# Optimization experiments

Hardware: AMD Instinct MI355X
Metric: run time of the kernel (lower is better)

Reference implementation:

```python
import jax, jax.numpy as jnp
import numpy as np

N0, N1, N2 = 100000, 20000, 4000
E0, E1 = 500000, 100000
D_IN, D_HID, D_OUT = 256, 256, 256


def setup_inputs() -> dict:
    key = jax.random.key(0)
    ks = jax.random.split(key, 12)
    s = 1.0 / np.sqrt(D_IN)
    return {
        "x": jax.random.normal(ks[0], (N0, D_IN), jnp.float32),
        "src0": jax.random.randint(ks[1], (E0,), 0, N0, jnp.int32),
        "dst0": jax.random.randint(ks[2], (E0,), 0, N1, jnp.int32),
        "w0": jax.random.uniform(ks[3], (E0,), jnp.float32),
        "src1": jax.random.randint(ks[4], (E1,), 0, N1, jnp.int32),
        "dst1": jax.random.randint(ks[5], (E1,), 0, N2, jnp.int32),
        "w1": jax.random.uniform(ks[6], (E1,), jnp.float32),
        "Wp1": jax.random.normal(ks[7], (D_IN, D_IN), jnp.float32) * s,
        "bp1": jnp.zeros((D_IN,), jnp.float32),
        "Ws1": jax.random.normal(ks[8], (D_IN, D_HID), jnp.float32) * s,
        "Wn1": jax.random.normal(ks[9], (D_IN, D_HID), jnp.float32) * s,
        "b1": jnp.zeros((D_HID,), jnp.float32),
        "Wp2": jax.random.normal(ks[10], (D_HID, D_HID), jnp.float32) * s,
        "bp2": jnp.zeros((D_HID,), jnp.float32),
        "Ws2": jax.random.normal(ks[11], (D_HID, D_OUT), jnp.float32) * s,
        "Wn2": jax.random.normal(jax.random.fold_in(key, 99), (D_HID, D_OUT), jnp.float32) * s,
        "b2": jnp.zeros((D_OUT,), jnp.float32),
    }


def sage_pool(x_src, src, dst, w, Wp, bp, Ws, Wn, b, n_dst):
    # DGL SAGEConv 'pool': relu(fc_pool(src feats)), edge-weighted msg, max reduce
    h = jax.nn.relu(x_src @ Wp + bp)          # [Nsrc, d]
    msg = h[src] * w[:, None]                 # [E, d] gather + edge weight
    agg = jax.ops.segment_max(msg, dst, num_segments=n_dst)
    agg = jnp.where(jnp.isfinite(agg), agg, 0.0)  # zero for isolated dst nodes
    x_dst = x_src[:n_dst]                     # block convention: dst = first n_dst src
    return x_dst @ Ws + agg @ Wn + b


def reference(x, src0, dst0, w0, src1, dst1, w1,
              Wp1, bp1, Ws1, Wn1, b1, Wp2, bp2, Ws2, Wn2, b2):
    h = sage_pool(x, src0, dst0, w0, Wp1, bp1, Ws1, Wn1, b1, N1)
    h = jax.nn.relu(h)
    h = sage_pool(h, src1, dst1, w1, Wp2, bp2, Ws2, Wn2, b2, N2)
    return jax.nn.relu(h)
```

## Files before the change

### kernel.cpp

```cpp
#include <hip/hip_runtime.h>
#include <hip/hip_bf16.h>

#define D 256
#define N0C 100000
#define N1C 20000
#define N2C 4000
#define BCAP 64
#define OVFCAP 4096

typedef short s16x8 __attribute__((ext_vector_type(8)));
typedef float f32x4 __attribute__((ext_vector_type(4)));

typedef __attribute__((address_space(3))) void lds_v;
typedef __attribute__((address_space(1))) void glb_v;

__device__ __forceinline__ short f2bf(float f) {
  __hip_bfloat16 b = __float2bfloat16(f);
  union { __hip_bfloat16 h; short s; } u;
  u.h = b;
  return u.s;
}
__device__ __forceinline__ float bf2f(short s) {
  return __uint_as_float(((unsigned)(unsigned short)s) << 16);
}

__global__ __launch_bounds__(256) void wtransp_k(
    const float* __restrict__ W0, const float* __restrict__ W1,
    const float* __restrict__ W2, const float* __restrict__ W3,
    const float* __restrict__ W4, const float* __restrict__ W5,
    short* __restrict__ T0, short* __restrict__ T1, short* __restrict__ T2,
    short* __restrict__ T3, short* __restrict__ T4, short* __restrict__ T5,
    int* __restrict__ ctrs, int nctr)
{
  int flat = (blockIdx.y * gridDim.x + blockIdx.x) * 256 + threadIdx.x;
  if (flat < nctr) ctrs[flat] = 0;

  const float* Ws[6] = {W0, W1, W2, W3, W4, W5};
  short* Ts[6] = {T0, T1, T2, T3, T4, T5};
  int g = blockIdx.y;
  int c = blockIdx.x * 256 + threadIdx.x;
  int lane = c & 63, kc = (c >> 6) & 7, g16 = c >> 9;
  int col = g16 * 16 + (lane & 15);
  int kbase = kc * 32 + (lane >> 4) * 8;
  const float* W = Ws[g];
  s16x8 o;
#pragma unroll
  for (int j = 0; j < 8; ++j) o[j] = f2bf(W[(size_t)(kbase + j) * D + col]);
  *(s16x8*)(Ts[g] + (size_t)c * 8) = o;
}

__global__ __launch_bounds__(256) void scat_direct_k(
    const int* __restrict__ src0, const int* __restrict__ dst0,
    const float* __restrict__ w0, int E0, int* __restrict__ cur0,
    int2* __restrict__ rec0, int* __restrict__ ovfc0, int4* __restrict__ ovf0,
    const int* __restrict__ src1, const int* __restrict__ dst1,
    const float* __restrict__ w1, int E1, int* __restrict__ cur1,
    int2* __restrict__ rec1, int* __restrict__ ovfc1, int4* __restrict__ ovf1)
{
  int i = blockIdx.x * 256 + threadIdx.x;
  if (i < E0) {
    int d = dst0[i];
    int p = atomicAdd(&cur0[d], 1);
    if (p < BCAP) rec0[d * BCAP + p] = make_int2(src0[i], __float_as_int(w0[i]));
    else {
      int q = atomicAdd(ovfc0, 1);
      if (q < OVFCAP) ovf0[q] = make_int4(d, src0[i], __float_as_int(w0[i]), 0);
    }
  } else if (i < E0 + E1) {
    int j = i - E0;
    int d = dst1[j];
    int p = atomicAdd(&cur1[d], 1);
    if (p < BCAP) rec1[d * BCAP + p] = make_int2(src1[j], __float_as_int(w1[j]));
    else {
      int q = atomicAdd(ovfc1, 1);
      if (q < OVFCAP) ovf1[q] = make_int4(d, src1[j], __float_as_int(w1[j]), 0);
    }
  }
}

__global__ __launch_bounds__(256) void seg_max_k(
    const short* __restrict__ h, const int* __restrict__ cur,
    const int2* __restrict__ rec, const int* __restrict__ ovfc,
    const int4* __restrict__ ovf, short* __restrict__ agg, int ndst)
{
  int dst = blockIdx.x * 4 + (threadIdx.x >> 6);
  if (dst >= ndst) return;
  int lane = threadIdx.x & 63;
  int cnt = cur[dst];
  cnt = cnt < BCAP ? cnt : BCAP;
  const int2* bp = rec + (size_t)dst * BCAP;
  const short* hp = h + (size_t)lane * 4;
  float m[8][4];
#pragma unroll
  for (int j = 0; j < 8; j++)
#pragma unroll
    for (int d2 = 0; d2 < 4; d2++) m[j][d2] = 0.f;
  int i = 0;
  for (; i + 7 < cnt; i += 8) {
    int2 r[8];
    short4 hv[8];
#pragma unroll
    for (int j = 0; j < 8; ++j) r[j] = bp[i + j];
#pragma unroll
    for (int j = 0; j < 8; ++j) hv[j] = *(const short4*)(hp + (size_t)r[j].x * D);
#pragma unroll
    for (int j = 0; j < 8; ++j) {
      float w = __int_as_float(r[j].y);
      m[j][0] = fmaxf(m[j][0], bf2f(hv[j].x) * w);
      m[j][1] = fmaxf(m[j][1], bf2f(hv[j].y) * w);
      m[j][2] = fmaxf(m[j][2], bf2f(hv[j].z) * w);
      m[j][3] = fmaxf(m[j][3], bf2f(hv[j].w) * w);
    }
  }
  for (; i < cnt; ++i) {
    int2 r0 = bp[i];
    short4 h0 = *(const short4*)(hp + (size_t)r0.x * D);
    float w0 = __int_as_float(r0.y);
    m[0][0] = fmaxf(m[0][0], bf2f(h0.x) * w0); m[0][1] = fmaxf(m[0][1], bf2f(h0.y) * w0);
    m[0][2] = fmaxf(m[0][2], bf2f(h0.z) * w0); m[0][3] = fmaxf(m[0][3], bf2f(h0.w) * w0);
  }
  int novf = *ovfc;
  novf = novf < OVFCAP ? novf : OVFCAP;
  for (int k = 0; k < novf; ++k) {
    int4 e = ovf[k];
    if (e.x == dst) {
      short4 h0 = *(const short4*)(hp + (size_t)e.y * D);
      float w0 = __int_as_float(e.z);
      m[0][0] = fmaxf(m[0][0], bf2f(h0.x) * w0); m[0][1] = fmaxf(m[0][1], bf2f(h0.y) * w0);
      m[0][2] = fmaxf(m[0][2], bf2f(h0.z) * w0); m[0][3] = fmaxf(m[0][3], bf2f(h0.w) * w0);
    }
  }
#pragma unroll
  for (int j = 1; j < 8; ++j)
#pragma unroll
    for (int d2 = 0; d2 < 4; d2++) m[0][d2] = fmaxf(m[0][d2], m[j][d2]);
  short4 o;
  o.x = f2bf(m[0][0]); o.y = f2bf(m[0][1]);
  o.z = f2bf(m[0][2]); o.w = f2bf(m[0][3]);
  *(short4*)(agg + (size_t)dst * D + lane * 4) = o;
}

__global__ __launch_bounds__(256, 2) void gemm1_k(
    const float* __restrict__ X, const short* __restrict__ Bp,
    const float* __restrict__ bias, short* __restrict__ out, int M)
{
  __shared__ float smem[64 * 256];
  const int tid = threadIdx.x;
  const int wave = tid >> 6, lane = tid & 63;
  const int lr = lane & 15, kg = lane >> 4;
  const int m_base = blockIdx.x * 64;

#pragma unroll
  for (int it = 0; it < 16; ++it) {
    int L = it * 4096 + tid * 16;
    int row = L >> 10;
    int colb = (L & 1023) ^ ((row & 7) << 4);
    int grow = m_base + row;
    grow = grow < M ? grow : M - 1;
    const char* gp = (const char*)X + (size_t)grow * 1024 + colb;
    char* lp = (char*)smem + L;
    __builtin_amdgcn_global_load_lds((const glb_v*)gp, (lds_v*)lp, 16, 0, 0);
  }
  __builtin_amdgcn_sched_barrier(0);

  s16x8 breg[4][8];
#pragma unroll
  for (int u = 0; u < 4; ++u)
#pragma unroll
    for (int kc = 0; kc < 8; ++kc) {
      int g16 = wave * 4 + u;
      breg[u][kc] = *(const s16x8*)(Bp + ((size_t)((g16 * 8 + kc) * 64 + lane)) * 8);
    }
  float bv[4];
#pragma unroll
  for (int u = 0; u < 4; ++u) bv[u] = bias[wave * 64 + u * 16 + lr];

  asm volatile("s_waitcnt vmcnt(32)" ::: "memory");
  __builtin_amdgcn_s_barrier();
  __builtin_amdgcn_sched_barrier(0);

  f32x4 acc[4][4];
#pragma unroll
  for (int t = 0; t < 4; t++)
#pragma unroll
    for (int u = 0; u < 4; u++) acc[t][u] = (f32x4)(0.0f);

#pragma unroll
  for (int kc = 0; kc < 8; ++kc) {
    s16x8 a[4];
#pragma unroll
    for (int t = 0; t < 4; ++t) {
      int row = t * 16 + lr;
      int base = (row << 10) + kc * 128 + kg * 32;
      int swz = (row & 7) << 4;
      f32x4 lo = *(const f32x4*)((const char*)smem + ((base) ^ swz));
      f32x4 hi = *(const f32x4*)((const char*)smem + ((base + 16) ^ swz));
      a[t][0] = f2bf(lo[0]); a[t][1] = f2bf(lo[1]);
      a[t][2] = f2bf(lo[2]); a[t][3] = f2bf(lo[3]);
      a[t][4] = f2bf(hi[0]); a[t][5] = f2bf(hi[1]);
      a[t][6] = f2bf(hi[2]); a[t][7] = f2bf(hi[3]);
    }
#pragma unroll
    for (int t = 0; t < 4; ++t)
#pragma unroll
      for (int u = 0; u < 4; ++u)
        acc[t][u] = __builtin_amdgcn_mfma_f32_16x16x32_bf16(a[t], breg[u][kc], acc[t][u], 0, 0, 0);
  }

#pragma unroll
  for (int t = 0; t < 4; ++t) {
    if (m_base + t * 16 < M) {
      int grow0 = m_base + t * 16 + kg * 4;
#pragma unroll
      for (int u = 0; u < 4; ++u) {
        int col = wave * 64 + u * 16 + lr;
#pragma unroll
        for (int i = 0; i < 4; ++i) {
          float v = acc[t][u][i] + bv[u];
          v = v > 0.0f ? v : 0.0f;
          out[(size_t)(grow0 + i) * D + col] = f2bf(v);
        }
      }
    }
  }
}

template<int F32OUT>
__global__ __launch_bounds__(256, 2) void gemm2s_k(
    const short* __restrict__ A1, const short* __restrict__ B1p,
    const short* __restrict__ A2, const short* __restrict__ B2p,
    const float* __restrict__ bias, void* __restrict__ outp, int M)
{
  __shared__ short smem[2 * 64 * 256];
  const int tid = threadIdx.x;
  const int wave = tid >> 6, lane = tid & 63;
  const int lr = lane & 15, kg = lane >> 4;
  const int m_base = blockIdx.x * 64;

  const short* As[2] = {A1, A2};
  const short* Bs[2] = {B1p, B2p};

#pragma unroll
  for (int s = 0; s < 2; ++s) {
#pragma unroll
    for (int it = 0; it < 8; ++it) {
      int L = it * 4096 + tid * 16;
      int row = L >> 9;
      int colb = (L & 511) ^ ((row & 7) << 4);
      int grow = m_base + row;
      grow = grow < M ? grow : M - 1;
      const char* gp = (const char*)As[s] + (size_t)grow * 512 + colb;
      char* lp = (char*)smem + s * 32768 + L;
      __builtin_amdgcn_global_load_lds((const glb_v*)gp, (lds_v*)lp, 16, 0, 0);
    }
  }
  __builtin_amdgcn_sched_barrier(0);

  f32x4 acc[4][4];
#pragma unroll
  for (int t = 0; t < 4; t++)
#pragma unroll
    for (int u = 0; u < 4; u++) acc[t][u] = (f32x4)(0.0f);

#pragma unroll
  for (int s = 0; s < 2; ++s) {
    s16x8 breg[4][8];
#pragma unroll
    for (int u = 0; u < 4; ++u)
#pragma unroll
      for (int kc = 0; kc < 8; ++kc) {
        int g16 = wave * 4 + u;
        breg[u][kc] = *(const s16x8*)(Bs[s] + ((size_t)((g16 * 8 + kc) * 64 + lane)) * 8);
      }
    if (s == 0) {
      asm volatile("s_waitcnt vmcnt(32)" ::: "memory");
      __builtin_amdgcn_s_barrier();
      __builtin_amdgcn_sched_barrier(0);
    }
#pragma unroll
    for (int kc = 0; kc < 8; ++kc) {
      s16x8 a[4];
#pragma unroll
      for (int t = 0; t < 4; ++t) {
        int row = t * 16 + lr;
        int base = (row << 9) + kc * 64 + kg * 16;
        int off = s * 32768 + (base ^ ((row & 7) << 4));
        a[t] = *(const s16x8*)((const char*)smem + off);
      }
#pragma unroll
      for (int t = 0; t < 4; ++t)
#pragma unroll
        for (int u = 0; u < 4; ++u)
          acc[t][u] = __builtin_amdgcn_mfma_f32_16x16x32_bf16(a[t], breg[u][kc], acc[t][u], 0, 0, 0);
    }
  }

#pragma unroll
  for (int t = 0; t < 4; ++t) {
    int grow0 = m_base + t * 16 + kg * 4;
    if (m_base + t * 16 < M) {
#pragma unroll
      for (int u = 0; u < 4; ++u) {
        int col = wave * 64 + u * 16 + lr;
        float bvv = bias[col];
#pragma unroll
        for (int i = 0; i < 4; ++i) {
          float v = acc[t][u][i] + bvv;
          v = v > 0.0f ? v : 0.0f;
          size_t idx = (size_t)(grow0 + i) * D + col;
          if (F32OUT) ((float*)outp)[idx] = v;
          else        ((short*)outp)[idx] = f2bf(v);
        }
      }
    }
  }
}

__global__ __launch_bounds__(256, 2) void gemm23_k(
    const float* __restrict__ X, const short* __restrict__ Bs1,
    const short* __restrict__ A2, const short* __restrict__ Bn1,
    const short* __restrict__ Bp2,
    const float* __restrict__ b1, const float* __restrict__ bp2,
    short* __restrict__ l1o, short* __restrict__ h2, int M, int LROWS)
{
  __shared__ short smem[2 * 64 * 256];
  const int tid = threadIdx.x;
  const int wave = tid >> 6, lane = tid & 63;
  const int lr = lane & 15, kg = lane >> 4;
  const int m_base = blockIdx.x * 64;

  const short* Bs[2] = {Bs1, Bn1};

#pragma unroll
  for (int it = 0; it < 8; ++it) {
    int L = it * 4096 + tid * 16;
    int row = L >> 9;
    int colb = (L & 511) ^ ((row & 7) << 4);
    int grow = m_base + row;
    grow = grow < M ? grow : M - 1;
    const char* gp = (const char*)A2 + (size_t)grow * 512 + colb;
    char* lp = (char*)smem + 32768 + L;
    __builtin_amdgcn_global_load_lds((const glb_v*)gp, (lds_v*)lp, 16, 0, 0);
  }
  __builtin_amdgcn_sched_barrier(0);

  {
    float4 fa[8][2];
#pragma unroll
    for (int it = 0; it < 8; ++it) {
      int L = it * 4096 + tid * 16;
      int row = L >> 9;
      int colel = (L & 511) >> 1;
      int grow = m_base + row;
      grow = grow < M ? grow : M - 1;
      const float* gp = X + (size_t)grow * D + colel;
      fa[it][0] = *(const float4*)gp;
      fa[it][1] = *(const float4*)(gp + 4);
    }
#pragma unroll
    for (int it = 0; it < 8; ++it) {
      int L = it * 4096 + tid * 16;
      int row = L >> 9;
      int Lw = L ^ ((row & 7) << 4);
      s16x8 o;
      o[0] = f2bf(fa[it][0].x); o[1] = f2bf(fa[it][0].y);
      o[2] = f2bf(fa[it][0].z); o[3] = f2bf(fa[it][0].w);
      o[4] = f2bf(fa[it][1].x); o[5] = f2bf(fa[it][1].y);
      o[6] = f2bf(fa[it][1].z); o[7] = f2bf(fa[it][1].w);
      *(s16x8*)((char*)smem + Lw) = o;
    }
    __builtin_amdgcn_sched_barrier(0);
  }

  f32x4 acc[4][4];
#pragma unroll
  for (int t = 0; t < 4; t++)
#pragma unroll
    for (int u = 0; u < 4; u++) acc[t][u] = (f32x4)(0.0f);

#pragma unroll
  for (int s = 0; s < 2; ++s) {
    s16x8 breg[4][8];
#pragma unroll
    for (int u = 0; u < 4; ++u)
#pragma unroll
      for (int kc = 0; kc < 8; ++kc) {
        int g16 = wave * 4 + u;
        breg[u][kc] = *(const s16x8*)(Bs[s] + ((size_t)((g16 * 8 + kc) * 64 + lane)) * 8);
      }
    if (s == 0) {
      __syncthreads();
      __builtin_amdgcn_sched_barrier(0);
    }
#pragma unroll
    for (int kc = 0; kc < 8; ++kc) {
      s16x8 a[4];
#pragma unroll
      for (int t = 0; t < 4; ++t) {
        int row = t * 16 + lr;
        int base = (row << 9) + kc * 64 + kg * 16;
        int off = s * 32768 + (base ^ ((row & 7) << 4));
        a[t] = *(const s16x8*)((const char*)smem + off);
      }
#pragma unroll
      for (int t = 0; t < 4; ++t)
#pragma unroll
        for (int u = 0; u < 4; ++u)
          acc[t][u] = __builtin_amdgcn_mfma_f32_16x16x32_bf16(a[t], breg[u][kc], acc[t][u], 0, 0, 0);
    }
  }

  __builtin_amdgcn_s_barrier();
  __builtin_amdgcn_sched_barrier(0);

  s16x8 breg2[4][8];
#pragma unroll
  for (int u = 0; u < 4; ++u)
#pragma unroll
    for (int kc = 0; kc < 8; ++kc) {
      int g16 = wave * 4 + u;
      breg2[u][kc] = *(const s16x8*)(Bp2 + ((size_t)((g16 * 8 + kc) * 64 + lane)) * 8);
    }

#pragma unroll
  for (int t = 0; t < 4; ++t)
#pragma unroll
    for (int u = 0; u < 4; ++u) {
      int col = wave * 64 + u * 16 + lr;
      float bvv = b1[col];
#pragma unroll
      for (int i = 0; i < 4; ++i) {
        int r = t * 16 + kg * 4 + i;
        float v = acc[t][u][i] + bvv;
        v = v > 0.0f ? v : 0.0f;
        short sv = f2bf(v);
        int grow = m_base + r;
        if (grow < LROWS) l1o[(size_t)grow * D + col] = sv;
        int ba = ((r << 9) + 2 * col) ^ ((r & 7) << 4);
        *(short*)((char*)smem + ba) = sv;
      }
    }
  asm volatile("s_waitcnt lgkmcnt(0)" ::: "memory");
  __builtin_amdgcn_s_barrier();
  __builtin_amdgcn_sched_barrier(0);

  f32x4 acc2[4][4];
#pragma unroll
  for (int t = 0; t < 4; t++)
#pragma unroll
    for (int u = 0; u < 4; u++) acc2[t][u] = (f32x4)(0.0f);
#pragma unroll
  for (int kc = 0; kc < 8; ++kc) {
    s16x8 a[4];
#pragma unroll
    for (int t = 0; t < 4; ++t) {
      int row = t * 16 + lr;
      int base = (row << 9) + kc * 64 + kg * 16;
      int off = base ^ ((row & 7) << 4);
      a[t] = *(const s16x8*)((const char*)smem + off);
    }
#pragma unroll
    for (int t = 0; t < 4; ++t)
#pragma unroll
      for (int u = 0; u < 4; ++u)
        acc2[t][u] = __builtin_amdgcn_mfma_f32_16x16x32_bf16(a[t], breg2[u][kc], acc2[t][u], 0, 0, 0);
  }

#pragma unroll
  for (int t = 0; t < 4; ++t) {
    int grow0 = m_base + t * 16 + kg * 4;
    if (m_base + t * 16 < M) {
#pragma unroll
      for (int u = 0; u < 4; ++u) {
        int col = wave * 64 + u * 16 + lr;
        float bvv = bp2[col];
#pragma unroll
        for (int i = 0; i < 4; ++i) {
          float v = acc2[t][u][i] + bvv;
          v = v > 0.0f ? v : 0.0f;
          h2[(size_t)(grow0 + i) * D + col] = f2bf(v);
        }
      }
    }
  }
}

extern "C" void kernel_launch(void* const* d_in, const int* in_sizes, int n_in,
                              void* d_out, int out_size, void* d_ws, size_t ws_size,
                              hipStream_t stream)
{
  const float* x    = (const float*)d_in[0];
  const int*   src0 = (const int*)d_in[1];
  const int*   dst0 = (const int*)d_in[2];
  const float* w0   = (const float*)d_in[3];
  const int*   src1 = (const int*)d_in[4];
  const int*   dst1 = (const int*)d_in[5];
  const float* w1   = (const float*)d_in[6];
  const float* Wp1  = (const float*)d_in[7];
  const float* bp1  = (const float*)d_in[8];
  const float* Ws1  = (const float*)d_in[9];
  const float* Wn1  = (const float*)d_in[10];
  const float* b1   = (const float*)d_in[11];
  const float* Wp2  = (const float*)d_in[12];
  const float* bp2  = (const float*)d_in[13];
  const float* Ws2  = (const float*)d_in[14];
  const float* Wn2  = (const float*)d_in[15];
  const float* b2   = (const float*)d_in[16];

  const int E0 = in_sizes[1], E1 = in_sizes[4];
  const int NCTR = N1C + N2C + 2;

  char* ws = (char*)d_ws;
  size_t off = 0;
  auto alloc = [&](size_t bytes) {
    void* p = ws + off;
    off += (bytes + 255) & ~(size_t)255;
    return p;
  };
  short* wp1t = (short*)alloc((size_t)D * D * 2);
  short* ws1t = (short*)alloc((size_t)D * D * 2);
  short* wn1t = (short*)alloc((size_t)D * D * 2);
  short* wp2t = (short*)alloc((size_t)D * D * 2);
  short* ws2t = (short*)alloc((size_t)D * D * 2);
  short* wn2t = (short*)alloc((size_t)D * D * 2);
  short* h1   = (short*)alloc((size_t)N0C * D * 2);
  short* h2   = (short*)alloc((size_t)N1C * D * 2);
  short* l1o  = (short*)alloc((size_t)N2C * D * 2);
  short* agg1 = (short*)alloc((size_t)N1C * D * 2);
  short* agg2 = (short*)alloc((size_t)N2C * D * 2);
  int*   ctrs = (int*)alloc((size_t)NCTR * 4);
  int*   cur0 = ctrs;
  int*   cur1 = ctrs + N1C;
  int*   ovfc0 = ctrs + N1C + N2C;
  int*   ovfc1 = ctrs + N1C + N2C + 1;
  int2*  rec0 = (int2*)alloc((size_t)N1C * BCAP * 8);
  int2*  rec1 = (int2*)alloc((size_t)N2C * BCAP * 8);
  int4*  ovf0 = (int4*)alloc((size_t)OVFCAP * 16);
  int4*  ovf1 = (int4*)alloc((size_t)OVFCAP * 16);

  wtransp_k<<<dim3(32, 6), 256, 0, stream>>>(Wp1, Ws1, Wn1, Wp2, Ws2, Wn2,
                                             wp1t, ws1t, wn1t, wp2t, ws2t, wn2t,
                                             ctrs, NCTR);

  int eb = (E0 + E1 + 255) / 256;
  scat_direct_k<<<eb, 256, 0, stream>>>(src0, dst0, w0, E0, cur0, rec0, ovfc0, ovf0,
                                        src1, dst1, w1, E1, cur1, rec1, ovfc1, ovf1);

  gemm1_k<<<(N0C + 63) / 64, 256, 0, stream>>>(x, wp1t, bp1, h1, N0C);
  seg_max_k<<<(N1C + 3) / 4, 256, 0, stream>>>(h1, cur0, rec0, ovfc0, ovf0, agg1, N1C);
  gemm23_k<<<(N1C + 63) / 64, 256, 0, stream>>>(
      x, ws1t, agg1, wn1t, wp2t, b1, bp2, l1o, h2, N1C, N2C);
  seg_max_k<<<(N2C + 3) / 4, 256, 0, stream>>>(h2, cur1, rec1, ovfc1, ovf1, agg2, N2C);
  gemm2s_k<1><<<(N2C + 63) / 64, 256, 0, stream>>>(
      l1o, ws2t, agg2, wn2t, b2, d_out, N2C);
}
```

Baseline: 163.0 us.

## Halve gemm1 row tile and async-load fp32 X into LDS in gemm23

```diff
diff --git a/kernel.cpp b/kernel.cpp
--- a/kernel.cpp
+++ b/kernel.cpp
@@ -140,18 +140,18 @@
   *(short4*)(agg + (size_t)dst * D + lane * 4) = o;
 }
 
-__global__ __launch_bounds__(256, 2) void gemm1_k(
+__global__ __launch_bounds__(256, 4) void gemm1_k(
     const float* __restrict__ X, const short* __restrict__ Bp,
     const float* __restrict__ bias, short* __restrict__ out, int M)
 {
-  __shared__ float smem[64 * 256];
+  __shared__ float smem[32 * 256];
   const int tid = threadIdx.x;
   const int wave = tid >> 6, lane = tid & 63;
   const int lr = lane & 15, kg = lane >> 4;
-  const int m_base = blockIdx.x * 64;
-
-#pragma unroll
-  for (int it = 0; it < 16; ++it) {
+  const int m_base = blockIdx.x * 32;
+
+#pragma unroll
+  for (int it = 0; it < 8; ++it) {
     int L = it * 4096 + tid * 16;
     int row = L >> 10;
     int colb = (L & 1023) ^ ((row & 7) << 4);
@@ -175,21 +175,21 @@
 #pragma unroll
   for (int u = 0; u < 4; ++u) bv[u] = bias[wave * 64 + u * 16 + lr];
 
-  asm volatile("s_waitcnt vmcnt(32)" ::: "memory");
+  asm volatile("s_waitcnt vmcnt(36)" ::: "memory");
   __builtin_amdgcn_s_barrier();
   __builtin_amdgcn_sched_barrier(0);
 
-  f32x4 acc[4][4];
-#pragma unroll
-  for (int t = 0; t < 4; t++)
+  f32x4 acc[2][4];
+#pragma unroll
+  for (int t = 0; t < 2; t++)
 #pragma unroll
     for (int u = 0; u < 4; u++) acc[t][u] = (f32x4)(0.0f);
 
 #pragma unroll
   for (int kc = 0; kc < 8; ++kc) {
-    s16x8 a[4];
-#pragma unroll
-    for (int t = 0; t < 4; ++t) {
+    s16x8 a[2];
+#pragma unroll
+    for (int t = 0; t < 2; ++t) {
       int row = t * 16 + lr;
       int base = (row << 10) + kc * 128 + kg * 32;
       int swz = (row & 7) << 4;
@@ -201,14 +201,14 @@
       a[t][6] = f2bf(hi[2]); a[t][7] = f2bf(hi[3]);
     }
 #pragma unroll
-    for (int t = 0; t < 4; ++t)
+    for (int t = 0; t < 2; ++t)
 #pragma unroll
       for (int u = 0; u < 4; ++u)
         acc[t][u] = __builtin_amdgcn_mfma_f32_16x16x32_bf16(a[t], breg[u][kc], acc[t][u], 0, 0, 0);
   }
 
 #pragma unroll
-  for (int t = 0; t < 4; ++t) {
+  for (int t = 0; t < 2; ++t) {
     if (m_base + t * 16 < M) {
       int grow0 = m_base + t * 16 + kg * 4;
 #pragma unroll
@@ -316,21 +316,31 @@
   }
 }
 
-__global__ __launch_bounds__(256, 2) void gemm23_k(
+__global__ __launch_bounds__(256, 1) void gemm23_k(
     const float* __restrict__ X, const short* __restrict__ Bs1,
     const short* __restrict__ A2, const short* __restrict__ Bn1,
     const short* __restrict__ Bp2,
     const float* __restrict__ b1, const float* __restrict__ bp2,
     short* __restrict__ l1o, short* __restrict__ h2, int M, int LROWS)
 {
-  __shared__ short smem[2 * 64 * 256];
+  __shared__ float smemf[24576];
+  char* smem = (char*)smemf;
   const int tid = threadIdx.x;
   const int wave = tid >> 6, lane = tid & 63;
   const int lr = lane & 15, kg = lane >> 4;
   const int m_base = blockIdx.x * 64;
 
-  const short* Bs[2] = {Bs1, Bn1};
-
+#pragma unroll
+  for (int it = 0; it < 16; ++it) {
+    int L = it * 4096 + tid * 16;
+    int row = L >> 10;
+    int colb = (L & 1023) ^ ((row & 7) << 4);
+    int grow = m_base + row;
+    grow = grow < M ? grow : M - 1;
+    const char* gp = (const char*)X + (size_t)grow * 1024 + colb;
+    char* lp = smem + L;
+    __builtin_amdgcn_global_load_lds((const glb_v*)gp, (lds_v*)lp, 16, 0, 0);
+  }
 #pragma unroll
   for (int it = 0; it < 8; ++it) {
     int L = it * 4096 + tid * 16;
@@ -339,38 +349,22 @@
     int grow = m_base + row;
     grow = grow < M ? grow : M - 1;
     const char* gp = (const char*)A2 + (size_t)grow * 512 + colb;
-    char* lp = (char*)smem + 32768 + L;
+    char* lp = smem + 65536 + L;
     __builtin_amdgcn_global_load_lds((const glb_v*)gp, (lds_v*)lp, 16, 0, 0);
   }
   __builtin_amdgcn_sched_barrier(0);
 
-  {
-    float4 fa[8][2];
-#pragma unroll
-    for (int it = 0; it < 8; ++it) {
-      int L = it * 4096 + tid * 16;
-      int row = L >> 9;
-      int colel = (L & 511) >> 1;
-      int grow = m_base + row;
-      grow = grow < M ? grow : M - 1;
-      const float* gp = X + (size_t)grow * D + colel;
-      fa[it][0] = *(const float4*)gp;
-      fa[it][1] = *(const float4*)(gp + 4);
-    }
-#pragma unroll
-    for (int it = 0; it < 8; ++it) {
-      int L = it * 4096 + tid * 16;
-      int row = L >> 9;
-      int Lw = L ^ ((row & 7) << 4);
-      s16x8 o;
-      o[0] = f2bf(fa[it][0].x); o[1] = f2bf(fa[it][0].y);
-      o[2] = f2bf(fa[it][0].z); o[3] = f2bf(fa[it][0].w);
-      o[4] = f2bf(fa[it][1].x); o[5] = f2bf(fa[it][1].y);
-      o[6] = f2bf(fa[it][1].z); o[7] = f2bf(fa[it][1].w);
-      *(s16x8*)((char*)smem + Lw) = o;
-    }
-    __builtin_amdgcn_sched_barrier(0);
-  }
+  s16x8 breg[4][8];
+#pragma unroll
+  for (int u = 0; u < 4; ++u)
+#pragma unroll
+    for (int kc = 0; kc < 8; ++kc) {
+      int g16 = wave * 4 + u;
+      breg[u][kc] = *(const s16x8*)(Bs1 + ((size_t)((g16 * 8 + kc) * 64 + lane)) * 8);
+    }
+  asm volatile("s_waitcnt vmcnt(32)" ::: "memory");
+  __builtin_amdgcn_s_barrier();
+  __builtin_amdgcn_sched_barrier(0);
 
   f32x4 acc[4][4];
 #pragma unroll
@@ -379,35 +373,49 @@
     for (int u = 0; u < 4; u++) acc[t][u] = (f32x4)(0.0f);
 
 #pragma unroll
-  for (int s = 0; s < 2; ++s) {
-    s16x8 breg[4][8];
-#pragma unroll
-    for (int u = 0; u < 4; ++u)
-#pragma unroll
-      for (int kc = 0; kc < 8; ++kc) {
-        int g16 = wave * 4 + u;
-        breg[u][kc] = *(const s16x8*)(Bs[s] + ((size_t)((g16 * 8 + kc) * 64 + lane)) * 8);
-      }
-    if (s == 0) {
-      __syncthreads();
-      __builtin_amdgcn_sched_barrier(0);
-    }
+  for (int kc = 0; kc < 8; ++kc) {
+    s16x8 a[4];
+#pragma unroll
+    for (int t = 0; t < 4; ++t) {
+      int row = t * 16 + lr;
+      int base = (row << 10) + kc * 128 + kg * 32;
+      int swz = (row & 7) << 4;
+      f32x4 lo = *(const f32x4*)(smem + ((base) ^ swz));
+      f32x4 hi = *(const f32x4*)(smem + ((base + 16) ^ swz));
+      a[t][0] = f2bf(lo[0]); a[t][1] = f2bf(lo[1]);
+      a[t][2] = f2bf(lo[2]); a[t][3] = f2bf(lo[3]);
+      a[t][4] = f2bf(hi[0]); a[t][5] = f2bf(hi[1]);
+      a[t][6] = f2bf(hi[2]); a[t][7] = f2bf(hi[3]);
+    }
+#pragma unroll
+    for (int t = 0; t < 4; ++t)
+#pragma unroll
+      for (int u = 0; u < 4; ++u)
+        acc[t][u] = __builtin_amdgcn_mfma_f32_16x16x32_bf16(a[t], breg[u][kc], acc[t][u], 0, 0, 0);
+  }
+
+#pragma unroll
+  for (int u = 0; u < 4; ++u)
 #pragma unroll
     for (int kc = 0; kc < 8; ++kc) {
-      s16x8 a[4];
-#pragma unroll
-      for (int t = 0; t < 4; ++t) {
-        int row = t * 16 + lr;
-        int base = (row << 9) + kc * 64 + kg * 16;
-        int off = s * 32768 + (base ^ ((row & 7) << 4));
-        a[t] = *(const s16x8*)((const char*)smem + off);
-      }
-#pragma unroll
-      for (int t = 0; t < 4; ++t)
-#pragma unroll
-        for (int u = 0; u < 4; ++u)
-          acc[t][u] = __builtin_amdgcn_mfma_f32_16x16x32_bf16(a[t], breg[u][kc], acc[t][u], 0, 0, 0);
-    }
+      int g16 = wave * 4 + u;
+      breg[u][kc] = *(const s16x8*)(Bn1 + ((size_t)((g16 * 8 + kc) * 64 + lane)) * 8);
+    }
+#pragma unroll
+  for (int kc = 0; kc < 8; ++kc) {
+    s16x8 a[4];
+#pragma unroll
+    for (int t = 0; t < 4; ++t) {
+      int row = t * 16 + lr;
+      int base = (row << 9) + kc * 64 + kg * 16;
+      int off = 65536 + (base ^ ((row & 7) << 4));
+      a[t] = *(const s16x8*)(smem + off);
+    }
+#pragma unroll
+    for (int t = 0; t < 4; ++t)
+#pragma unroll
+      for (int u = 0; u < 4; ++u)
+        acc[t][u] = __builtin_amdgcn_mfma_f32_16x16x32_bf16(a[t], breg[u][kc], acc[t][u], 0, 0, 0);
   }
 
   __builtin_amdgcn_s_barrier();
@@ -437,7 +445,7 @@
         int grow = m_base + r;
         if (grow < LROWS) l1o[(size_t)grow * D + col] = sv;
         int ba = ((r << 9) + 2 * col) ^ ((r & 7) << 4);
-        *(short*)((char*)smem + ba) = sv;
+        *(short*)(smem + ba) = sv;
       }
     }
   asm volatile("s_waitcnt lgkmcnt(0)" ::: "memory");
@@ -457,7 +465,7 @@
       int row = t * 16 + lr;
       int base = (row << 9) + kc * 64 + kg * 16;
       int off = base ^ ((row & 7) << 4);
-      a[t] = *(const s16x8*)((const char*)smem + off);
+      a[t] = *(const s16x8*)(smem + off);
     }
 #pragma unroll
     for (int t = 0; t < 4; ++t)
@@ -546,7 +554,7 @@
   scat_direct_k<<<eb, 256, 0, stream>>>(src0, dst0, w0, E0, cur0, rec0, ovfc0, ovf0,
                                         src1, dst1, w1, E1, cur1, rec1, ovfc1, ovf1);
 
-  gemm1_k<<<(N0C + 63) / 64, 256, 0, stream>>>(x, wp1t, bp1, h1, N0C);
+  gemm1_k<<<(N0C + 31) / 32, 256, 0, stream>>>(x, wp1t, bp1, h1, N0C);
   seg_max_k<<<(N1C + 3) / 4, 256, 0, stream>>>(h1, cur0, rec0, ovfc0, ovf0, agg1, N1C);
   gemm23_k<<<(N1C + 63) / 64, 256, 0, stream>>>(
       x, ws1t, agg1, wn1t, wp2t, b1, bp2, l1o, h2, N1C, N2C);
```

New measurement: 203.6 us. 24.9% more time.

## Make gemm1 persistent with double-buffered LDS prefetch of 32-row tiles

Applied to the files above, without the earlier changes.

```diff
diff --git a/kernel.cpp b/kernel.cpp
--- a/kernel.cpp
+++ b/kernel.cpp
@@ -140,27 +140,33 @@
   *(short4*)(agg + (size_t)dst * D + lane * 4) = o;
 }
 
+__device__ __forceinline__ void stage1_tile(const float* __restrict__ X,
+                                            float* smem, int t, int buf,
+                                            int tid, int M) {
+#pragma unroll
+  for (int it = 0; it < 8; ++it) {
+    int L = it * 4096 + tid * 16;
+    int row = L >> 10;
+    int colb = (L & 1023) ^ ((row & 7) << 4);
+    int grow = t * 32 + row;
+    grow = grow < M ? grow : M - 1;
+    const char* gp = (const char*)X + (size_t)grow * 1024 + colb;
+    char* lp = (char*)smem + buf * 32768 + L;
+    __builtin_amdgcn_global_load_lds((const glb_v*)gp, (lds_v*)lp, 16, 0, 0);
+  }
+}
+
 __global__ __launch_bounds__(256, 2) void gemm1_k(
     const float* __restrict__ X, const short* __restrict__ Bp,
-    const float* __restrict__ bias, short* __restrict__ out, int M)
-{
-  __shared__ float smem[64 * 256];
+    const float* __restrict__ bias, short* __restrict__ out,
+    int M, int T, int G)
+{
+  __shared__ float smem[2 * 32 * 256];
   const int tid = threadIdx.x;
   const int wave = tid >> 6, lane = tid & 63;
   const int lr = lane & 15, kg = lane >> 4;
-  const int m_base = blockIdx.x * 64;
-
-#pragma unroll
-  for (int it = 0; it < 16; ++it) {
-    int L = it * 4096 + tid * 16;
-    int row = L >> 10;
-    int colb = (L & 1023) ^ ((row & 7) << 4);
-    int grow = m_base + row;
-    grow = grow < M ? grow : M - 1;
-    const char* gp = (const char*)X + (size_t)grow * 1024 + colb;
-    char* lp = (char*)smem + L;
-    __builtin_amdgcn_global_load_lds((const glb_v*)gp, (lds_v*)lp, 16, 0, 0);
-  }
+
+  stage1_tile(X, smem, blockIdx.x, 0, tid, M);
   __builtin_amdgcn_sched_barrier(0);
 
   s16x8 breg[4][8];
@@ -175,53 +181,68 @@
 #pragma unroll
   for (int u = 0; u < 4; ++u) bv[u] = bias[wave * 64 + u * 16 + lr];
 
-  asm volatile("s_waitcnt vmcnt(32)" ::: "memory");
-  __builtin_amdgcn_s_barrier();
-  __builtin_amdgcn_sched_barrier(0);
-
-  f32x4 acc[4][4];
-#pragma unroll
-  for (int t = 0; t < 4; t++)
-#pragma unroll
-    for (int u = 0; u < 4; u++) acc[t][u] = (f32x4)(0.0f);
-
-#pragma unroll
-  for (int kc = 0; kc < 8; ++kc) {
-    s16x8 a[4];
-#pragma unroll
-    for (int t = 0; t < 4; ++t) {
-      int row = t * 16 + lr;
-      int base = (row << 10) + kc * 128 + kg * 32;
-      int swz = (row & 7) << 4;
-      f32x4 lo = *(const f32x4*)((const char*)smem + ((base) ^ swz));
-      f32x4 hi = *(const f32x4*)((const char*)smem + ((base + 16) ^ swz));
-      a[t][0] = f2bf(lo[0]); a[t][1] = f2bf(lo[1]);
-      a[t][2] = f2bf(lo[2]); a[t][3] = f2bf(lo[3]);
-      a[t][4] = f2bf(hi[0]); a[t][5] = f2bf(hi[1]);
-      a[t][6] = f2bf(hi[2]); a[t][7] = f2bf(hi[3]);
-    }
-#pragma unroll
-    for (int t = 0; t < 4; ++t)
-#pragma unroll
-      for (int u = 0; u < 4; ++u)
-        acc[t][u] = __builtin_amdgcn_mfma_f32_16x16x32_bf16(a[t], breg[u][kc], acc[t][u], 0, 0, 0);
-  }
-
-#pragma unroll
-  for (int t = 0; t < 4; ++t) {
-    if (m_base + t * 16 < M) {
-      int grow0 = m_base + t * 16 + kg * 4;
-#pragma unroll
-      for (int u = 0; u < 4; ++u) {
-        int col = wave * 64 + u * 16 + lr;
-#pragma unroll
-        for (int i = 0; i < 4; ++i) {
-          float v = acc[t][u][i] + bv[u];
-          v = v > 0.0f ? v : 0.0f;
-          out[(size_t)(grow0 + i) * D + col] = f2bf(v);
+  int bufc = 0;
+  for (int t = blockIdx.x; t < T; t += G) {
+    int tn = t + G;
+    if (tn < T) {
+      stage1_tile(X, smem, tn, bufc ^ 1, tid, M);
+      __builtin_amdgcn_sched_barrier(0);
+      asm volatile("s_waitcnt vmcnt(8)" ::: "memory");
+    } else {
+      asm volatile("s_waitcnt vmcnt(0)" ::: "memory");
+    }
+    __builtin_amdgcn_s_barrier();
+    __builtin_amdgcn_sched_barrier(0);
+
+    const char* sb = (const char*)smem + bufc * 32768;
+    f32x4 acc[2][4];
+#pragma unroll
+    for (int t2 = 0; t2 < 2; t2++)
+#pragma unroll
+      for (int u = 0; u < 4; u++) acc[t2][u] = (f32x4)(0.0f);
+
+#pragma unroll
+    for (int kc = 0; kc < 8; ++kc) {
+      s16x8 a[2];
+#pragma unroll
+      for (int t2 = 0; t2 < 2; ++t2) {
+        int row = t2 * 16 + lr;
+        int base = (row << 10) + kc * 128 + kg * 32;
+        int swz = (row & 7) << 4;
+        f32x4 lo = *(const f32x4*)(sb + ((base) ^ swz));
+        f32x4 hi = *(const f32x4*)(sb + ((base + 16) ^ swz));
+        a[t2][0] = f2bf(lo[0]); a[t2][1] = f2bf(lo[1]);
+        a[t2][2] = f2bf(lo[2]); a[t2][3] = f2bf(lo[3]);
+        a[t2][4] = f2bf(hi[0]); a[t2][5] = f2bf(hi[1]);
+        a[t2][6] = f2bf(hi[2]); a[t2][7] = f2bf(hi[3]);
+      }
+#pragma unroll
+      for (int t2 = 0; t2 < 2; ++t2)
+#pragma unroll
+        for (int u = 0; u < 4; ++u)
+          acc[t2][u] = __builtin_amdgcn_mfma_f32_16x16x32_bf16(a[t2], breg[u][kc], acc[t2][u], 0, 0, 0);
+    }
+
+    int m_base = t * 32;
+#pragma unroll
+    for (int t2 = 0; t2 < 2; ++t2) {
+      if (m_base + t2 * 16 < M) {
+        int grow0 = m_base + t2 * 16 + kg * 4;
+#pragma unroll
+        for (int u = 0; u < 4; ++u) {
+          int col = wave * 64 + u * 16 + lr;
+#pragma unroll
+          for (int i = 0; i < 4; ++i) {
+            float v = acc[t2][u][i] + bv[u];
+            v = v > 0.0f ? v : 0.0f;
+            out[(size_t)(grow0 + i) * D + col] = f2bf(v);
+          }
         }
       }
     }
+    __builtin_amdgcn_s_barrier();
+    __builtin_amdgcn_sched_barrier(0);
+    bufc ^= 1;
   }
 }
 
@@ -546,7 +567,8 @@
   scat_direct_k<<<eb, 256, 0, stream>>>(src0, dst0, w0, E0, cur0, rec0, ovfc0, ovf0,
                                         src1, dst1, w1, E1, cur1, rec1, ovfc1, ovf1);
 
-  gemm1_k<<<(N0C + 63) / 64, 256, 0, stream>>>(x, wp1t, bp1, h1, N0C);
+  const int T1 = (N0C + 31) / 32;
+  gemm1_k<<<512, 256, 0, stream>>>(x, wp1t, bp1, h1, N0C, T1, 512);
   seg_max_k<<<(N1C + 3) / 4, 256, 0, stream>>>(h1, cur0, rec0, ovfc0, ovf0, agg1, N1C);
   gemm23_k<<<(N1C + 63) / 64, 256, 0, stream>>>(
       x, ws1t, agg1, wn1t, wp2t, b1, bp2, l1o, h2, N1C, N2C);
```

New measurement: 156.6 us. -3.9%, faster.
